# Kernel optimization log

Hardware: AMD Instinct MI355X
Metric: run time of the kernel (lower is better)

Reference implementation:

```python
import jax, jax.numpy as jnp
import numpy as np

T = 10
CH, H, W = 16, 16, 264  # torch grid_sample sees view(1,16,16,264) as N,C,H,W
L, C = 256, 264


def _warp(img, pose):
    """Replicates F.affine_grid + F.grid_sample (bilinear, zeros padding,
    align_corners=False) on img of shape (CH,H,W) with pose=(dx,dy,dyaw)."""
    dx, dy, yaw = pose[0], pose[1], pose[2]
    cos, sin = jnp.cos(yaw), jnp.sin(yaw)
    # normalized base grid, align_corners=False: (2i+1)/N - 1
    xs = (2.0 * jnp.arange(W, dtype=img.dtype) + 1.0) / W - 1.0  # (W,)
    ys = (2.0 * jnp.arange(H, dtype=img.dtype) + 1.0) / H - 1.0  # (H,)
    gx = cos * xs[None, :] + sin * ys[:, None] + dx   # (H,W)
    gy = -sin * xs[None, :] + cos * ys[:, None] + dy  # (H,W)
    # unnormalize (align_corners=False)
    ix = ((gx + 1.0) * W - 1.0) * 0.5
    iy = ((gy + 1.0) * H - 1.0) * 0.5
    ix0 = jnp.floor(ix); iy0 = jnp.floor(iy)
    ix1 = ix0 + 1.0;     iy1 = iy0 + 1.0
    wx1 = ix - ix0; wx0 = 1.0 - wx1
    wy1 = iy - iy0; wy0 = 1.0 - wy1

    def gather(xf, yf):
        inb = (xf >= 0) & (xf < W) & (yf >= 0) & (yf < H)
        xi = jnp.clip(xf.astype(jnp.int32), 0, W - 1)
        yi = jnp.clip(yf.astype(jnp.int32), 0, H - 1)
        v = img[:, yi, xi]                      # (CH,H,W)
        return v * inb.astype(img.dtype)        # zero padding

    out = (gather(ix0, iy0) * (wx0 * wy0)
           + gather(ix1, iy0) * (wx1 * wy0)
           + gather(ix0, iy1) * (wx0 * wy1)
           + gather(ix1, iy1) * (wx1 * wy1))
    return out  # (CH,H,W)


def _forward(fuse_feature, delta_ego_pos):
    ff = fuse_feature                              # (10,256,264)
    dp = delta_ego_pos                             # (10,3)
    ff_sp = ff.reshape(T, CH, H, W)
    # prefix sums: P[k] = sum(dp[0:k]); cumulative pose for (b,t) = -sum(dp[t-1:b])
    P = jnp.concatenate([jnp.zeros((1, 3), dp.dtype), jnp.cumsum(dp, axis=0)], axis=0)
    bs = jnp.repeat(jnp.arange(T), T - 1)          # (90,) frame index
    ts = jnp.tile(jnp.arange(1, T), T)             # (90,) past-frame offset t in [1,9]
    poses = -(P[bs] - P[ts - 1])                   # (90,3)
    valid = (ts <= bs)                             # n_valid_past(b) = b
    src = ff_sp[ts]                                # (90,CH,H,W)
    warped = jax.vmap(_warp)(src, poses)           # (90,CH,H,W)
    warped = warped * valid[:, None, None, None].astype(ff.dtype)
    aligned = jnp.zeros((T, T, CH, H, W), ff.dtype)
    aligned = aligned.at[bs, (T - 1) - ts].set(warped)
    aligned = aligned.at[:, T - 1].set(ff_sp)      # current frame, unwarped
    # (B,T,L*C) self-attention fusion
    tb = aligned.reshape(T, T, L * C)
    scores = jnp.einsum('btd,bsd->bts', tb, tb)
    attn = jax.nn.softmax(scores, axis=-1)
    fused = jnp.einsum('bts,bsd->btd', attn, tb)
    fused = fused.mean(axis=1)                     # (B, L*C)
    return fused.reshape(T, L, C)                  # (10,256,264)


def setup_inputs() -> dict:
    key = jax.random.key(0)
    k1, k2 = jax.random.split(key)
    # scale features so the d=67584 dot products don't saturate the softmax
    fuse_feature = jax.random.normal(k1, (T, L, C), dtype=jnp.float32) * 0.02
    delta_ego_pos = jax.random.normal(k2, (T, 3), dtype=jnp.float32) * 0.1
    return {"fuse_feature": fuse_feature, "delta_ego_pos": delta_ego_pos}


def reference(fuse_feature, delta_ego_pos):
    return _forward(fuse_feature, delta_ego_pos)
```

## Files before the change

### kernel.cpp

```cpp
#include <hip/hip_runtime.h>
#include <math.h>

#define TT 10
#define CHN 16
#define HH 16
#define WW 264
#define HW (HH*WW)
#define DD (CHN*HW)
#define NCH 66
#define NACC 55


__device__ __forceinline__ void pose_setup(const float* __restrict__ dp, int b,
                                           float4* __restrict__ pose) {
    if (threadIdx.x < TT-1) {
        int ts = (int)threadIdx.x + 1;
        float ax = 0.f, ay = 0.f, az = 0.f;
        for (int j = 0; j < ts-1; ++j) { ax += dp[3*j]; ay += dp[3*j+1]; az += dp[3*j+2]; }
        float bx = 0.f, by = 0.f, bz = 0.f;
        for (int j = 0; j < b; ++j)    { bx += dp[3*j]; by += dp[3*j+1]; bz += dp[3*j+2]; }
        float yaw = az - bz;
        pose[threadIdx.x] = make_float4(ax - bx, ay - by,
                                        (float)cos((double)yaw), (float)sin((double)yaw));
    }
}

__device__ __forceinline__ void plan_slot(float xs, float ys, float4 m,
                                          int& o00, int& o10, int& o01, int& o11,
                                          float& w00, float& w10, float& w01, float& w11) {
    float gx =  m.z*xs + m.w*ys + m.x;
    float gy = -m.w*xs + m.z*ys + m.y;
    float ix = ((gx + 1.f)*(float)WW - 1.f)*0.5f;
    float iy = ((gy + 1.f)*(float)HH - 1.f)*0.5f;
    float ix0f = floorf(ix), iy0f = floorf(iy);
    float wx1 = ix - ix0f, wx0 = 1.f - wx1;
    float wy1 = iy - iy0f, wy0 = 1.f - wy1;
    int ix0 = (int)ix0f, iy0 = (int)iy0f;
    int ix1 = ix0 + 1,   iy1 = iy0 + 1;
    bool inx0 = (ix0 >= 0) && (ix0 < WW);
    bool inx1 = (ix1 >= 0) && (ix1 < WW);
    bool iny0 = (iy0 >= 0) && (iy0 < HH);
    bool iny1 = (iy1 >= 0) && (iy1 < HH);
    int xi0 = min(max(ix0, 0), WW-1), xi1 = min(max(ix1, 0), WW-1);
    int yi0 = min(max(iy0, 0), HH-1), yi1 = min(max(iy1, 0), HH-1);
    float wx0m = inx0 ? wx0 : 0.f, wx1m = inx1 ? wx1 : 0.f;
    float wy0m = iny0 ? wy0 : 0.f, wy1m = iny1 ? wy1 : 0.f;
    o00 = yi0*WW + xi0; o10 = yi0*WW + xi1;
    o01 = yi1*WW + xi0; o11 = yi1*WW + xi1;
    w00 = wx0m*wy0m; w10 = wx1m*wy0m;
    w01 = wx0m*wy1m; w11 = wx1m*wy1m;
}

__global__ __launch_bounds__(256) void gram_fused_kernel(const float* __restrict__ ff,
                                                         const float* __restrict__ dp,
                                                         float* __restrict__ scores,
                                                         int* __restrict__ cnt,
                                                         float* __restrict__ w) {
    int b = blockIdx.y;
    int lane = threadIdx.x & 63, wv = threadIdx.x >> 6;
    int p = blockIdx.x*64 + lane;
    __shared__ float4 pose[TT-1];
    pose_setup(dp, b, pose);
    __syncthreads();

    int y = p / WW, x = p - y*WW;
    float xs = (2.f*(float)x + 1.f)*(1.f/(float)WW) - 1.f;
    float ys = (2.f*(float)y + 1.f)*(1.f/(float)HH) - 1.f;

    float v[TT][4];
    #pragma unroll
    for (int s = 0; s < TT; ++s) {
        #pragma unroll
        for (int c = 0; c < 4; ++c) v[s][c] = 0.f;
        if (s == TT-1) {
            const float* src = ff + b*DD + (wv*4)*HW + p;
            #pragma unroll
            for (int c = 0; c < 4; ++c) v[s][c] = src[c*HW];
            continue;
        }
        int ts = (TT-1) - s;
        if (ts > b) continue;
        int o00,o10,o01,o11; float w00,w10,w01,w11;
        plan_slot(xs, ys, pose[ts-1], o00,o10,o01,o11, w00,w10,w01,w11);
        const float* src = ff + ts*DD + (wv*4)*HW;
        #pragma unroll
        for (int c = 0; c < 4; ++c) {
            const float* fc = src + c*HW;
            v[s][c] = fc[o00]*w00 + fc[o10]*w10 + fc[o01]*w01 + fc[o11]*w11;
        }
    }

    float acc[NACC];
    #pragma unroll
    for (int k = 0; k < NACC; ++k) acc[k] = 0.f;
    #pragma unroll
    for (int c = 0; c < 4; ++c) {
        int k = 0;
        #pragma unroll
        for (int t = 0; t < TT; ++t)
            #pragma unroll
            for (int s2 = t; s2 < TT; ++s2)
                acc[k++] += v[t][c]*v[s2][c];
    }

    __shared__ float red[NACC*4];
    #pragma unroll
    for (int k = 0; k < NACC; ++k) {
        float a = acc[k];
        #pragma unroll
        for (int o = 32; o > 0; o >>= 1) a += __shfl_down(a, o);
        if (lane == 0) red[k*4 + wv] = a;
    }
    __syncthreads();
    if (threadIdx.x < NACC) {
        float a = red[threadIdx.x*4] + red[threadIdx.x*4+1]
                + red[threadIdx.x*4+2] + red[threadIdx.x*4+3];
        atomicAdd(&scores[b*NACC + threadIdx.x], a);
    }
    __syncthreads();

    __shared__ int last;
    if (threadIdx.x == 0) {
        __threadfence();
        int old = __hip_atomic_fetch_add(&cnt[b], 1, __ATOMIC_ACQ_REL,
                                         __HIP_MEMORY_SCOPE_AGENT);
        last = (old == NCH - 1) ? 1 : 0;
    }
    __syncthreads();
    if (!last) return;

    __shared__ float sc[NACC];
    __shared__ float mx_l[TT], den_l[TT];
    if (threadIdx.x < NACC)
        sc[threadIdx.x] = __hip_atomic_load(&scores[b*NACC + threadIdx.x],
                                            __ATOMIC_ACQUIRE, __HIP_MEMORY_SCOPE_AGENT);
    __syncthreads();
    if (threadIdx.x < TT) {
        int t = threadIdx.x;
        float mx = -1e30f;
        #pragma unroll
        for (int s = 0; s < TT; ++s) {
            int a0 = min(t, s), a1 = max(t, s);
            mx = fmaxf(mx, sc[a0*TT - a0*(a0-1)/2 + (a1 - a0)]);
        }
        float den = 0.f;
        #pragma unroll
        for (int s = 0; s < TT; ++s) {
            int a0 = min(t, s), a1 = max(t, s);
            den += expf(sc[a0*TT - a0*(a0-1)/2 + (a1 - a0)] - mx);
        }
        mx_l[t] = mx; den_l[t] = den;
    }
    __syncthreads();
    if (threadIdx.x < TT) {
        int s = threadIdx.x;
        float acc2 = 0.f;
        #pragma unroll
        for (int t = 0; t < TT; ++t) {
            int a0 = min(t, s), a1 = max(t, s);
            acc2 += expf(sc[a0*TT - a0*(a0-1)/2 + (a1 - a0)] - mx_l[t]) / den_l[t];
        }
        w[b*TT + s] = acc2 * 0.1f;
    }
}

__global__ __launch_bounds__(256) void out_fused_kernel(const float* __restrict__ ff,
                                                        const float* __restrict__ dp,
                                                        const float* __restrict__ w,
                                                        float* __restrict__ out) {
    int b = blockIdx.y;
    int lane = threadIdx.x & 63, wv = threadIdx.x >> 6;
    int p = blockIdx.x*64 + lane;
    __shared__ float4 pose[TT-1];
    __shared__ float wl[TT];
    pose_setup(dp, b, pose);
    if (threadIdx.x < TT) wl[threadIdx.x] = w[b*TT + threadIdx.x];
    __syncthreads();

    int y = p / WW, x = p - y*WW;
    float xs = (2.f*(float)x + 1.f)*(1.f/(float)WW) - 1.f;
    float ys = (2.f*(float)y + 1.f)*(1.f/(float)HH) - 1.f;

    float o[4] = {0.f, 0.f, 0.f, 0.f};
    #pragma unroll
    for (int s = 0; s < TT; ++s) {
        if (s == TT-1) {
            float wb = wl[s];
            const float* src = ff + b*DD + (wv*4)*HW + p;
            #pragma unroll
            for (int c = 0; c < 4; ++c) o[c] += wb*src[c*HW];
            continue;
        }
        int ts = (TT-1) - s;
        if (ts > b) continue;
        int o00,o10,o01,o11; float w00,w10,w01,w11;
        plan_slot(xs, ys, pose[ts-1], o00,o10,o01,o11, w00,w10,w01,w11);
        float wb = wl[s];
        w00 *= wb; w10 *= wb; w01 *= wb; w11 *= wb;
        const float* src = ff + ts*DD + (wv*4)*HW;
        #pragma unroll
        for (int c = 0; c < 4; ++c) {
            const float* fc = src + c*HW;
            o[c] += fc[o00]*w00 + fc[o10]*w10 + fc[o01]*w01 + fc[o11]*w11;
        }
    }
    #pragma unroll
    for (int c = 0; c < 4; ++c)
        out[(size_t)b*DD + (wv*4 + c)*HW + p] = o[c];
}

extern "C" void kernel_launch(void* const* d_in, const int* in_sizes, int n_in,
                              void* d_out, int out_size, void* d_ws, size_t ws_size,
                              hipStream_t stream) {
    const float* ff = (const float*)d_in[0];
    const float* dp = (const float*)d_in[1];
    float* out = (float*)d_out;

    char* ws = (char*)d_ws;
    float* scores = (float*)ws;
    int*   cnt    = (int*)(ws + 2560);
    float* w      = (float*)(ws + 3072);

    hipMemsetAsync(ws, 0, 4096, stream);
    gram_fused_kernel<<<dim3(NCH, TT), 256, 0, stream>>>(ff, dp, scores, cnt, w);
    out_fused_kernel <<<dim3(NCH, TT), 256, 0, stream>>>(ff, dp, w, out);
}
```

Before: 99.25 us.

## Fuse gram and output kernels with intra-grid flag wait, keep warped values in registers

Merges the two kernels into one. The last-arriving block per batch computes the softmax weights and publishes a flag, and every block spin-waits on that flag before computing its output from the warped values it still holds in registers. This removes the second launch and the second round of bilinear gathers. It relies on all 660 blocks being co-resident, since the spin-wait can deadlock otherwise, and launch_bounds(256,3) is added to help that. A dummy float4 prefetch of ff is also added, with a never-taken store that keeps the load alive, apparently to warm the cache.

```diff
diff --git a/kernel.cpp b/kernel.cpp
--- a/kernel.cpp
+++ b/kernel.cpp
@@ -51,17 +51,27 @@
     w01 = wx0m*wy1m; w11 = wx1m*wy1m;
 }
 
-__global__ __launch_bounds__(256) void gram_fused_kernel(const float* __restrict__ ff,
-                                                         const float* __restrict__ dp,
-                                                         float* __restrict__ scores,
-                                                         int* __restrict__ cnt,
-                                                         float* __restrict__ w) {
+__global__ __launch_bounds__(256, 3) void fused_kernel(const float* __restrict__ ff,
+                                                       const float* __restrict__ dp,
+                                                       float* __restrict__ scores,
+                                                       int* __restrict__ cnt,
+                                                       int* __restrict__ flag,
+                                                       float* __restrict__ w,
+                                                       float* __restrict__ dummy,
+                                                       float* __restrict__ out) {
     int b = blockIdx.y;
     int lane = threadIdx.x & 63, wv = threadIdx.x >> 6;
     int p = blockIdx.x*64 + lane;
+
+    int g = (b*NCH + blockIdx.x)*256 + threadIdx.x;
+    float4 wf = ((const float4*)ff)[g];
+
     __shared__ float4 pose[TT-1];
     pose_setup(dp, b, pose);
     __syncthreads();
+
+    float wsum = wf.x + wf.y + wf.z + wf.w;
+    if (wsum == 1.2345678e-38f) dummy[threadIdx.x] = wsum;
 
     int y = p / WW, x = p - y*WW;
     float xs = (2.f*(float)x + 1.f)*(1.f/(float)WW) - 1.f;
@@ -127,82 +137,65 @@
         last = (old == NCH - 1) ? 1 : 0;
     }
     __syncthreads();
-    if (!last) return;
-
-    __shared__ float sc[NACC];
-    __shared__ float mx_l[TT], den_l[TT];
-    if (threadIdx.x < NACC)
-        sc[threadIdx.x] = __hip_atomic_load(&scores[b*NACC + threadIdx.x],
-                                            __ATOMIC_ACQUIRE, __HIP_MEMORY_SCOPE_AGENT);
-    __syncthreads();
-    if (threadIdx.x < TT) {
-        int t = threadIdx.x;
-        float mx = -1e30f;
-        #pragma unroll
-        for (int s = 0; s < TT; ++s) {
-            int a0 = min(t, s), a1 = max(t, s);
-            mx = fmaxf(mx, sc[a0*TT - a0*(a0-1)/2 + (a1 - a0)]);
-        }
-        float den = 0.f;
-        #pragma unroll
-        for (int s = 0; s < TT; ++s) {
-            int a0 = min(t, s), a1 = max(t, s);
-            den += expf(sc[a0*TT - a0*(a0-1)/2 + (a1 - a0)] - mx);
-        }
-        mx_l[t] = mx; den_l[t] = den;
-    }
-    __syncthreads();
-    if (threadIdx.x < TT) {
-        int s = threadIdx.x;
-        float acc2 = 0.f;
-        #pragma unroll
-        for (int t = 0; t < TT; ++t) {
-            int a0 = min(t, s), a1 = max(t, s);
-            acc2 += expf(sc[a0*TT - a0*(a0-1)/2 + (a1 - a0)] - mx_l[t]) / den_l[t];
-        }
-        w[b*TT + s] = acc2 * 0.1f;
-    }
-}
-
-__global__ __launch_bounds__(256) void out_fused_kernel(const float* __restrict__ ff,
-                                                        const float* __restrict__ dp,
-                                                        const float* __restrict__ w,
-                                                        float* __restrict__ out) {
-    int b = blockIdx.y;
-    int lane = threadIdx.x & 63, wv = threadIdx.x >> 6;
-    int p = blockIdx.x*64 + lane;
-    __shared__ float4 pose[TT-1];
+
+    if (last) {
+        __shared__ float sc[NACC];
+        __shared__ float mx_l[TT], den_l[TT];
+        if (threadIdx.x < NACC)
+            sc[threadIdx.x] = __hip_atomic_load(&scores[b*NACC + threadIdx.x],
+                                                __ATOMIC_ACQUIRE, __HIP_MEMORY_SCOPE_AGENT);
+        __syncthreads();
+        if (threadIdx.x < TT) {
+            int t = threadIdx.x;
+            float mx = -1e30f;
+            #pragma unroll
+            for (int s = 0; s < TT; ++s) {
+                int a0 = min(t, s), a1 = max(t, s);
+                mx = fmaxf(mx, sc[a0*TT - a0*(a0-1)/2 + (a1 - a0)]);
+            }
+            float den = 0.f;
+            #pragma unroll
+            for (int s = 0; s < TT; ++s) {
+                int a0 = min(t, s), a1 = max(t, s);
+                den += expf(sc[a0*TT - a0*(a0-1)/2 + (a1 - a0)] - mx);
+            }
+            mx_l[t] = mx; den_l[t] = den;
+        }
+        __syncthreads();
+        if (threadIdx.x < TT) {
+            int s = threadIdx.x;
+            float a2 = 0.f;
+            #pragma unroll
+            for (int t = 0; t < TT; ++t) {
+                int a0 = min(t, s), a1 = max(t, s);
+                a2 += expf(sc[a0*TT - a0*(a0-1)/2 + (a1 - a0)] - mx_l[t]) / den_l[t];
+            }
+            __hip_atomic_store(&w[b*TT + s], a2 * 0.1f, __ATOMIC_RELAXED,
+                               __HIP_MEMORY_SCOPE_AGENT);
+        }
+        __syncthreads();
+        if (threadIdx.x == 0)
+            __hip_atomic_store(&flag[b], 1, __ATOMIC_RELEASE, __HIP_MEMORY_SCOPE_AGENT);
+    }
+
+    if (threadIdx.x == 0) {
+        while (__hip_atomic_load(&flag[b], __ATOMIC_ACQUIRE,
+                                 __HIP_MEMORY_SCOPE_AGENT) == 0)
+            __builtin_amdgcn_s_sleep(4);
+    }
+    __syncthreads();
     __shared__ float wl[TT];
-    pose_setup(dp, b, pose);
-    if (threadIdx.x < TT) wl[threadIdx.x] = w[b*TT + threadIdx.x];
-    __syncthreads();
-
-    int y = p / WW, x = p - y*WW;
-    float xs = (2.f*(float)x + 1.f)*(1.f/(float)WW) - 1.f;
-    float ys = (2.f*(float)y + 1.f)*(1.f/(float)HH) - 1.f;
+    if (threadIdx.x < TT)
+        wl[threadIdx.x] = __hip_atomic_load(&w[b*TT + threadIdx.x], __ATOMIC_RELAXED,
+                                            __HIP_MEMORY_SCOPE_AGENT);
+    __syncthreads();
 
     float o[4] = {0.f, 0.f, 0.f, 0.f};
     #pragma unroll
     for (int s = 0; s < TT; ++s) {
-        if (s == TT-1) {
-            float wb = wl[s];
-            const float* src = ff + b*DD + (wv*4)*HW + p;
-            #pragma unroll
-            for (int c = 0; c < 4; ++c) o[c] += wb*src[c*HW];
-            continue;
-        }
-        int ts = (TT-1) - s;
-        if (ts > b) continue;
-        int o00,o10,o01,o11; float w00,w10,w01,w11;
-        plan_slot(xs, ys, pose[ts-1], o00,o10,o01,o11, w00,w10,w01,w11);
         float wb = wl[s];
-        w00 *= wb; w10 *= wb; w01 *= wb; w11 *= wb;
-        const float* src = ff + ts*DD + (wv*4)*HW;
-        #pragma unroll
-        for (int c = 0; c < 4; ++c) {
-            const float* fc = src + c*HW;
-            o[c] += fc[o00]*w00 + fc[o10]*w10 + fc[o01]*w01 + fc[o11]*w11;
-        }
+        #pragma unroll
+        for (int c = 0; c < 4; ++c) o[c] += wb*v[s][c];
     }
     #pragma unroll
     for (int c = 0; c < 4; ++c)
@@ -219,9 +212,11 @@
     char* ws = (char*)d_ws;
     float* scores = (float*)ws;
     int*   cnt    = (int*)(ws + 2560);
+    int*   flag   = (int*)(ws + 2688);
     float* w      = (float*)(ws + 3072);
+    float* dummy  = (float*)(ws + 4096);
 
     hipMemsetAsync(ws, 0, 4096, stream);
-    gram_fused_kernel<<<dim3(NCH, TT), 256, 0, stream>>>(ff, dp, scores, cnt, w);
-    out_fused_kernel <<<dim3(NCH, TT), 256, 0, stream>>>(ff, dp, w, out);
-}
+    fused_kernel<<<dim3(NCH, TT), 256, 0, stream>>>(ff, dp, scores, cnt, flag,
+                                                    w, dummy, out);
+}
```

Result: slower. 115.9 us (+16.8%).
